# Kernel optimization log

Hardware: AMD Instinct MI355X
Metric: run time of the kernel (lower is better)

The kernel has to match this reference:

```python
import jax, jax.numpy as jnp
import numpy as np

N = 100000   # nodes
E = 640000   # edges
D = 128      # feature dim
G = 512      # graphs in the batch


def setup_inputs() -> dict:
    key = jax.random.key(0)
    ks = jax.random.split(key, 6)
    x = jax.random.normal(ks[0], (N, D), dtype=jnp.float32)
    edge_index = jax.random.randint(ks[1], (2, E), 0, N, dtype=jnp.int32)
    batch = jnp.sort(jax.random.randint(ks[2], (N,), 0, G, dtype=jnp.int32))
    scale = 1.0 / np.sqrt(D)
    W0 = jax.random.normal(ks[3], (D, D), dtype=jnp.float32) * scale
    W1 = jax.random.normal(ks[4], (D, D), dtype=jnp.float32) * scale
    W2 = jax.random.normal(ks[5], (D, D), dtype=jnp.float32) * scale
    return {"x": x, "edge_index": edge_index, "batch": batch,
            "W0": W0, "W1": W1, "W2": W2}


def gcn_conv(x, W, row, col, n):
    """GCNConv (bias=False): x' = D^-1/2 (A + I) D^-1/2 (x @ W).
    row/col already include self-loops."""
    xw = x @ W                                              # [N, D]
    deg = jax.ops.segment_sum(jnp.ones_like(col, dtype=x.dtype), col,
                              num_segments=n)               # [N]
    dinv = jnp.where(deg > 0, jax.lax.rsqrt(deg), 0.0)
    norm = dinv[row] * dinv[col]                            # [E+N]
    msgs = norm[:, None] * xw[row]                          # gather + scale
    return jax.ops.segment_sum(msgs, col, num_segments=n)   # scatter-add


def reference(x, edge_index, batch, W0, W1, W2):
    n = x.shape[0]
    loops = jnp.arange(n, dtype=edge_index.dtype)
    row = jnp.concatenate([edge_index[0], loops])
    col = jnp.concatenate([edge_index[1], loops])
    # conv_layers[:-1] (no activation between them in forward)
    x = gcn_conv(x, W0, row, col, n)
    x = gcn_conv(x, W1, row, col, n)
    x = jax.nn.leaky_relu(x, negative_slope=0.01)
    x = gcn_conv(x, W2, row, col, n)
    # global_add_pool over graph ids
    return jax.ops.segment_sum(x, batch, num_segments=G)    # [G, D]
```

## Files before the change

kernel.cpp:

```cpp
#include <hip/hip_runtime.h>
#include <hip/hip_bf16.h>

#define FEAT 128

typedef unsigned int uint32;
typedef unsigned long long uint64;
typedef unsigned short ushort16;
typedef __attribute__((ext_vector_type(8))) short short8;
typedef __attribute__((ext_vector_type(4))) float v4f;
typedef __attribute__((ext_vector_type(2))) float f32x2;

__device__ __forceinline__ ushort16 f2bf(float f) {
    uint32 u = __float_as_uint(f);
    u += 0x7fffu + ((u >> 16) & 1u);
    return (ushort16)(u >> 16);
}
__device__ __forceinline__ float bflo(uint32 u) { return __uint_as_float(u << 16); }
__device__ __forceinline__ float bfhi(uint32 u) { return __uint_as_float(u & 0xffff0000u); }
__device__ __forceinline__ f32x2 up2(uint32 u) { return (f32x2){bflo(u), bfhi(u)}; }

__global__ __launch_bounds__(256) void hydra_kernel(const float* __restrict__ x,
                                                    ushort16* __restrict__ Xh,
                                                    const int* __restrict__ col,
                                                    int* __restrict__ counts,
                                                    const float* __restrict__ W0,
                                                    const float* __restrict__ W1,
                                                    ushort16* __restrict__ W01t,
                                                    int cvtBlocks, int histBlocks,
                                                    int total8, int E) {
    int b = blockIdx.x;
    int t = threadIdx.x;
    if (b < cvtBlocks) {
        int id = b * 256 + t;
        if (id < total8) {
            const float4 v0 = *(const float4*)(x + (size_t)id * 8);
            const float4 v1 = *(const float4*)(x + (size_t)id * 8 + 4);
            uint4 o;
            o.x = (uint32)f2bf(v0.x) | ((uint32)f2bf(v0.y) << 16);
            o.y = (uint32)f2bf(v0.z) | ((uint32)f2bf(v0.w) << 16);
            o.z = (uint32)f2bf(v1.x) | ((uint32)f2bf(v1.y) << 16);
            o.w = (uint32)f2bf(v1.z) | ((uint32)f2bf(v1.w) << 16);
            *(uint4*)(Xh + (size_t)id * 8) = o;
        }
    } else if (b < cvtBlocks + histBlocks) {
        int id = (b - cvtBlocks) * 256 + t;
        if (id * 4 + 3 < E) {
            int4 c4 = *(const int4*)(col + id * 4);
            atomicAdd(&counts[c4.x], 1);
            atomicAdd(&counts[c4.y], 1);
            atomicAdd(&counts[c4.z], 1);
            atomicAdd(&counts[c4.w], 1);
        } else {
            for (int e = id * 4; e < E; e++) atomicAdd(&counts[col[e]], 1);
        }
    } else {
        __shared__ float sW0[2][FEAT];
        int wb = b - cvtBlocks - histBlocks;
        int lk = t >> 7;
        int ncol = t & 127;
        int k = wb * 2 + lk;
        sW0[lk][ncol] = W0[(size_t)k * FEAT + ncol];
        __syncthreads();
        float acc = 0.f;
#pragma unroll 4
        for (int j = 0; j < FEAT; j++)
            acc += sW0[lk][j] * W1[(size_t)j * FEAT + ncol];
        W01t[(size_t)ncol * FEAT + k] = f2bf(acc);
    }
}

__global__ __launch_bounds__(256) void scan_part(const int* __restrict__ counts,
                                                 int* __restrict__ bsum, int n) {
    __shared__ int s[256];
    int base = blockIdx.x * 1024;
    int t = threadIdx.x;
    int v = 0;
#pragma unroll
    for (int i = 0; i < 4; i++) {
        int idx = base + t * 4 + i;
        if (idx < n) v += counts[idx];
    }
    s[t] = v;
    __syncthreads();
    for (int o = 128; o > 0; o >>= 1) {
        if (t < o) s[t] += s[t + o];
        __syncthreads();
    }
    if (t == 0) bsum[blockIdx.x] = s[0];
}

__global__ void scan_bsum(int* __restrict__ bsum, int nb) {
    __shared__ int s[128];
    int t = threadIdx.x;
    int v0 = (t < nb) ? bsum[t] : 0;
    s[t] = v0;
    __syncthreads();
    for (int o = 1; o < 128; o <<= 1) {
        int v = (t >= o) ? s[t - o] : 0;
        __syncthreads();
        s[t] += v;
        __syncthreads();
    }
    if (t < nb) bsum[t] = s[t] - v0;
}

__global__ __launch_bounds__(256) void scan_final(const int* __restrict__ counts,
                                                  const int* __restrict__ bsum,
                                                  int* __restrict__ off, int* __restrict__ nxt,
                                                  float* __restrict__ dinv, int n) {
    __shared__ int s[256];
    int base = blockIdx.x * 1024;
    int t = threadIdx.x;
    int c[4];
    int sum = 0;
#pragma unroll
    for (int i = 0; i < 4; i++) {
        int idx = base + t * 4 + i;
        c[i] = (idx < n) ? counts[idx] : 0;
        sum += c[i];
    }
    int v0 = sum;
    s[t] = sum;
    __syncthreads();
    for (int o = 1; o < 256; o <<= 1) {
        int v = (t >= o) ? s[t - o] : 0;
        __syncthreads();
        s[t] += v;
        __syncthreads();
    }
    int excl = s[t] - v0 + bsum[blockIdx.x];
#pragma unroll
    for (int i = 0; i < 4; i++) {
        int idx = base + t * 4 + i;
        if (idx < n) {
            off[idx] = excl;
            nxt[idx] = excl;
            dinv[idx] = rsqrtf((float)(c[i] + 1));
        }
        excl += c[i];
    }
    if (blockIdx.x == gridDim.x - 1 && t == 255) off[n] = excl;
}

__global__ void fill_kernel(const int* __restrict__ row, const int* __restrict__ col,
                            const float* __restrict__ dinv, int* __restrict__ nxt,
                            uint64* __restrict__ erec, int E) {
    int e = blockIdx.x * 256 + threadIdx.x;
    if (e < E) {
        int c = col[e], r = row[e];
        int p = atomicAdd(&nxt[c], 1);
        uint64 v = (uint64)(uint32)r | ((uint64)__float_as_uint(dinv[r]) << 32);
        __builtin_nontemporal_store(v, &erec[p]);
    }
}

__global__ __launch_bounds__(256) void gemm_mfma(const ushort16* __restrict__ A,
                                                 const ushort16* __restrict__ Wt,
                                                 ushort16* __restrict__ Ch, int n,
                                                 int leaky) {
    const int t = threadIdx.x;
    const int w = t >> 6;
    const int lane = t & 63;
    const int quad = lane >> 4;
    const int l16 = lane & 15;
    const int colBase = (w & 1) * 64;

    short8 wf[4][4];
#pragma unroll
    for (int ct = 0; ct < 4; ct++) {
        const ushort16* wp = Wt + (size_t)(colBase + ct * 16 + l16) * FEAT + quad * 8;
#pragma unroll
        for (int ks = 0; ks < 4; ks++) wf[ct][ks] = *(const short8*)(wp + ks * 32);
    }

    const int nTiles = (n + 15) >> 4;
    const int tStride = gridDim.x * 2;
    int tile = blockIdx.x * 2 + (w >> 1);
    if (tile >= nTiles) return;

    auto loadA = [&](int tl, short8 (&a)[4]) {
        const int row = tl * 16 + l16;
        if (row < n) {
            const ushort16* ap = A + (size_t)row * FEAT + quad * 8;
#pragma unroll
            for (int ks = 0; ks < 4; ks++) a[ks] = *(const short8*)(ap + ks * 32);
        } else {
#pragma unroll
            for (int ks = 0; ks < 4; ks++) a[ks] = (short8)0;
        }
    };

    short8 aCur[4];
    loadA(tile, aCur);

    while (tile < nTiles) {
        const int nextTile = tile + tStride;
        short8 aNxt[4];
        if (nextTile < nTiles) loadA(nextTile, aNxt);

        v4f acc[4];
#pragma unroll
        for (int ct = 0; ct < 4; ct++) acc[ct] = (v4f)0.f;
#pragma unroll
        for (int ct = 0; ct < 4; ct++)
#pragma unroll
            for (int ks = 0; ks < 4; ks++)
                acc[ct] = __builtin_amdgcn_mfma_f32_16x16x32_bf16(wf[ct][ks], aCur[ks], acc[ct], 0, 0, 0);

        const int row = tile * 16 + l16;
        if (row < n) {
#pragma unroll
            for (int ct = 0; ct < 4; ct++) {
                float p0 = acc[ct][0], p1 = acc[ct][1], p2 = acc[ct][2], p3 = acc[ct][3];
                if (leaky) {
                    p0 = (p0 >= 0.f) ? p0 : 0.01f * p0;
                    p1 = (p1 >= 0.f) ? p1 : 0.01f * p1;
                    p2 = (p2 >= 0.f) ? p2 : 0.01f * p2;
                    p3 = (p3 >= 0.f) ? p3 : 0.01f * p3;
                }
                uint2 o;
                o.x = (uint32)f2bf(p0) | ((uint32)f2bf(p1) << 16);
                o.y = (uint32)f2bf(p2) | ((uint32)f2bf(p3) << 16);
                *(uint2*)(Ch + (size_t)row * FEAT + colBase + ct * 16 + quad * 4) = o;
            }
        }

        tile = nextTile;
#pragma unroll
        for (int ks = 0; ks < 4; ks++) aCur[ks] = aNxt[ks];
    }
}

__global__ __launch_bounds__(256) void gather_kernel(const int* __restrict__ off,
                                                     const uint2* __restrict__ erec,
                                                     const float* __restrict__ dinv,
                                                     const ushort16* __restrict__ XWh,
                                                     ushort16* __restrict__ Hh, int n) {
    int node = blockIdx.x * 4 + (threadIdx.x >> 6);
    if (node >= n) return;
    int lane = threadIdx.x & 63;
    int grp = lane >> 4;
    int l16 = lane & 15;
    float dc = dinv[node];
    const uint4* table = (const uint4*)XWh;

    f32x2 acc[4];
    if (grp == 0) {
        uint4 v = table[(size_t)node * 16 + l16];
        f32x2 w0 = (f32x2){dc * dc, dc * dc};
        acc[0] = w0 * up2(v.x);
        acc[1] = w0 * up2(v.y);
        acc[2] = w0 * up2(v.z);
        acc[3] = w0 * up2(v.w);
    } else {
#pragma unroll
        for (int j = 0; j < 4; j++) acc[j] = (f32x2){0.f, 0.f};
    }

    int s = off[node], e = off[node + 1];
    int i = s + grp;
    for (; i + 4 < e; i += 8) {
        uint2 er0 = erec[i];
        uint2 er1 = erec[i + 4];
        uint4 u0 = table[(size_t)er0.x * 16 + l16];
        uint4 u1 = table[(size_t)er1.x * 16 + l16];
        float f0 = dc * __uint_as_float(er0.y);
        float f1 = dc * __uint_as_float(er1.y);
        f32x2 n0 = (f32x2){f0, f0};
        f32x2 n1 = (f32x2){f1, f1};
        acc[0] += n0 * up2(u0.x);
        acc[1] += n0 * up2(u0.y);
        acc[2] += n0 * up2(u0.z);
        acc[3] += n0 * up2(u0.w);
        acc[0] += n1 * up2(u1.x);
        acc[1] += n1 * up2(u1.y);
        acc[2] += n1 * up2(u1.z);
        acc[3] += n1 * up2(u1.w);
    }
    if (i < e) {
        uint2 er0 = erec[i];
        uint4 u0 = table[(size_t)er0.x * 16 + l16];
        float f0 = dc * __uint_as_float(er0.y);
        f32x2 n0 = (f32x2){f0, f0};
        acc[0] += n0 * up2(u0.x);
        acc[1] += n0 * up2(u0.y);
        acc[2] += n0 * up2(u0.z);
        acc[3] += n0 * up2(u0.w);
    }

    float b[8] = {acc[0].x, acc[0].y, acc[1].x, acc[1].y,
                  acc[2].x, acc[2].y, acc[3].x, acc[3].y};
#pragma unroll
    for (int j = 0; j < 8; j++) {
        b[j] += __shfl_xor(b[j], 16);
        b[j] += __shfl_xor(b[j], 32);
    }

    if (grp == 0) {
        uint4 o;
        o.x = (uint32)f2bf(b[0]) | ((uint32)f2bf(b[1]) << 16);
        o.y = (uint32)f2bf(b[2]) | ((uint32)f2bf(b[3]) << 16);
        o.z = (uint32)f2bf(b[4]) | ((uint32)f2bf(b[5]) << 16);
        o.w = (uint32)f2bf(b[6]) | ((uint32)f2bf(b[7]) << 16);
        *(uint4*)(Hh + (size_t)node * FEAT + l16 * 8) = o;
    }
}

__global__ __launch_bounds__(128) void pool_kernel(const ushort16* __restrict__ H,
                                                   const int* __restrict__ batch,
                                                   float* __restrict__ P, int n) {
    int t = threadIdx.x;
    int i0 = blockIdx.x * 64;
    if (i0 >= n) return;
    int i1 = min(i0 + 64, n);
    float acc = 0.f;
    int g = batch[i0];
    for (int i = i0; i < i1; i++) {
        int b = batch[i];
        if (b != g) {
            atomicAdd(&P[(size_t)g * FEAT + t], acc);
            acc = 0.f;
            g = b;
        }
        uint32 u = (uint32)(unsigned short)H[(size_t)i * FEAT + t];
        acc += __uint_as_float(u << 16);
    }
    atomicAdd(&P[(size_t)g * FEAT + t], acc);
}

__global__ __launch_bounds__(128) void pgemm_kernel(const float* __restrict__ P,
                                                    const float* __restrict__ W2,
                                                    float* __restrict__ out) {
    __shared__ float sP[FEAT];
    const int g = blockIdx.x;
    const int t = threadIdx.x;
    sP[t] = P[(size_t)g * FEAT + t];
    __syncthreads();
    float o = 0.f;
#pragma unroll 4
    for (int k = 0; k < FEAT; k++) o += sP[k] * W2[(size_t)k * FEAT + t];
    out[(size_t)g * FEAT + t] = o;
}

extern "C" void kernel_launch(void* const* d_in, const int* in_sizes, int n_in,
                              void* d_out, int out_size, void* d_ws, size_t ws_size,
                              hipStream_t stream) {
    const float* x = (const float*)d_in[0];
    const int* ei = (const int*)d_in[1];
    const int* batch = (const int*)d_in[2];
    const float* W0 = (const float*)d_in[3];
    const float* W1 = (const float*)d_in[4];
    const float* W2 = (const float*)d_in[5];
    float* out = (float*)d_out;

    const int N = in_sizes[0] / FEAT;
    const int E = in_sizes[1] / 2;
    const int G = out_size / FEAT;

    const int* rowI = ei;
    const int* colI = ei + E;

    char* ws = (char*)d_ws;
    auto take = [&](size_t bytes) {
        char* p = ws;
        ws += (bytes + 15) & ~(size_t)15;
        return p;
    };
    int* counts    = (int*)take((size_t)N * 4);
    int* off       = (int*)take((size_t)(N + 1) * 4);
    int* nxt       = (int*)take((size_t)N * 4);
    float* dinv    = (float*)take((size_t)N * 4);
    int* bsum      = (int*)take(128 * 4);
    uint64* erec   = (uint64*)take((size_t)E * 8);
    ushort16* W01t = (ushort16*)take((size_t)16384 * 2);
    float* Pbuf    = (float*)take((size_t)G * FEAT * 4);
    ushort16* Xh   = (ushort16*)take((size_t)N * FEAT * 2);
    ushort16* bufA = (ushort16*)take((size_t)N * FEAT * 2);
    ushort16* bufB = (ushort16*)take((size_t)N * FEAT * 2);

    const int nb = (N + 1023) / 1024;
    const int eb = (E + 255) / 256;

    hipMemsetAsync(counts, 0, (size_t)N * 4, stream);
    hipMemsetAsync(Pbuf, 0, (size_t)G * FEAT * 4, stream);
    const int total8 = N * FEAT / 8;
    const int cvtBlocks = (total8 + 255) / 256;
    const int histBlocks = (E + 1023) / 1024;
    hydra_kernel<<<cvtBlocks + histBlocks + 64, 256, 0, stream>>>(
        x, Xh, colI, counts, W0, W1, W01t, cvtBlocks, histBlocks, total8, E);

    scan_part<<<nb, 256, 0, stream>>>(counts, bsum, N);
    scan_bsum<<<1, 128, 0, stream>>>(bsum, nb);
    scan_final<<<nb, 256, 0, stream>>>(counts, bsum, off, nxt, dinv, N);
    fill_kernel<<<eb, 256, 0, stream>>>(rowI, colI, dinv, nxt, erec, E);

    const int gatBlocks = (N + 3) / 4;

    gather_kernel<<<gatBlocks, 256, 0, stream>>>(off, (const uint2*)erec, dinv, Xh, bufA, N);
    gather_kernel<<<gatBlocks, 256, 0, stream>>>(off, (const uint2*)erec, dinv, bufA, bufB, N);
    gemm_mfma<<<1024, 256, 0, stream>>>(bufB, W01t, bufA, N, 1);
    gather_kernel<<<gatBlocks, 256, 0, stream>>>(off, (const uint2*)erec, dinv, bufA, bufB, N);
    pool_kernel<<<(N + 63) / 64, 128, 0, stream>>>(bufB, batch, Pbuf, N);
    pgemm_kernel<<<G, 128, 0, stream>>>(Pbuf, W2, out);
}
```

Baseline: 373.6 us.

## Drop scan_bsum and Pbuf memset launches, store source-only edge records

Folds the Pbuf zeroing into extra blocks of the hydra kernel, which removes a memset. It also removes the scan_bsum kernel by having each scan_final block sum the preceding block totals from shared memory. The edge records shrink from 8-byte (source, dinv) pairs to 4-byte source indices, and the gather kernels now read dinv[src] with a separate random load. This cuts kernel launches and halves edge-record traffic, at the cost of an extra dependent gather per edge in each of the three gather passes.

```diff
diff --git a/kernel.cpp b/kernel.cpp
--- a/kernel.cpp
+++ b/kernel.cpp
@@ -26,6 +26,7 @@
                                                     const float* __restrict__ W0,
                                                     const float* __restrict__ W1,
                                                     ushort16* __restrict__ W01t,
+                                                    float* __restrict__ Pbuf,
                                                     int cvtBlocks, int histBlocks,
                                                     int total8, int E) {
     int b = blockIdx.x;
@@ -53,7 +54,7 @@
         } else {
             for (int e = id * 4; e < E; e++) atomicAdd(&counts[col[e]], 1);
         }
-    } else {
+    } else if (b < cvtBlocks + histBlocks + 64) {
         __shared__ float sW0[2][FEAT];
         int wb = b - cvtBlocks - histBlocks;
         int lk = t >> 7;
@@ -66,6 +67,12 @@
         for (int j = 0; j < FEAT; j++)
             acc += sW0[lk][j] * W1[(size_t)j * FEAT + ncol];
         W01t[(size_t)ncol * FEAT + k] = f2bf(acc);
+    } else {
+        int zb = b - cvtBlocks - histBlocks - 64;
+        float4 z = make_float4(0.f, 0.f, 0.f, 0.f);
+        float* p = Pbuf + (size_t)zb * 2048 + t * 8;
+        *(float4*)p = z;
+        *(float4*)(p + 4) = z;
     }
 }
 
@@ -89,28 +96,15 @@
     if (t == 0) bsum[blockIdx.x] = s[0];
 }
 
-__global__ void scan_bsum(int* __restrict__ bsum, int nb) {
-    __shared__ int s[128];
-    int t = threadIdx.x;
-    int v0 = (t < nb) ? bsum[t] : 0;
-    s[t] = v0;
-    __syncthreads();
-    for (int o = 1; o < 128; o <<= 1) {
-        int v = (t >= o) ? s[t - o] : 0;
-        __syncthreads();
-        s[t] += v;
-        __syncthreads();
-    }
-    if (t < nb) bsum[t] = s[t] - v0;
-}
-
 __global__ __launch_bounds__(256) void scan_final(const int* __restrict__ counts,
                                                   const int* __restrict__ bsum,
                                                   int* __restrict__ off, int* __restrict__ nxt,
-                                                  float* __restrict__ dinv, int n) {
+                                                  float* __restrict__ dinv, int n, int nb) {
     __shared__ int s[256];
+    __shared__ int sb[128];
     int base = blockIdx.x * 1024;
     int t = threadIdx.x;
+    if (t < nb) sb[t] = bsum[t];
     int c[4];
     int sum = 0;
 #pragma unroll
@@ -128,7 +122,9 @@
         s[t] += v;
         __syncthreads();
     }
-    int excl = s[t] - v0 + bsum[blockIdx.x];
+    int blockBase = 0;
+    for (int j = 0; j < blockIdx.x; j++) blockBase += sb[j];
+    int excl = s[t] - v0 + blockBase;
 #pragma unroll
     for (int i = 0; i < 4; i++) {
         int idx = base + t * 4 + i;
@@ -143,14 +139,13 @@
 }
 
 __global__ void fill_kernel(const int* __restrict__ row, const int* __restrict__ col,
-                            const float* __restrict__ dinv, int* __restrict__ nxt,
-                            uint64* __restrict__ erec, int E) {
+                            int* __restrict__ nxt,
+                            int* __restrict__ srcArr, int E) {
     int e = blockIdx.x * 256 + threadIdx.x;
     if (e < E) {
         int c = col[e], r = row[e];
         int p = atomicAdd(&nxt[c], 1);
-        uint64 v = (uint64)(uint32)r | ((uint64)__float_as_uint(dinv[r]) << 32);
-        __builtin_nontemporal_store(v, &erec[p]);
+        __builtin_nontemporal_store(r, &srcArr[p]);
     }
 }
 
@@ -232,7 +227,7 @@
 }
 
 __global__ __launch_bounds__(256) void gather_kernel(const int* __restrict__ off,
-                                                     const uint2* __restrict__ erec,
+                                                     const int* __restrict__ srcArr,
                                                      const float* __restrict__ dinv,
                                                      const ushort16* __restrict__ XWh,
                                                      ushort16* __restrict__ Hh, int n) {
@@ -260,12 +255,12 @@
     int s = off[node], e = off[node + 1];
     int i = s + grp;
     for (; i + 4 < e; i += 8) {
-        uint2 er0 = erec[i];
-        uint2 er1 = erec[i + 4];
-        uint4 u0 = table[(size_t)er0.x * 16 + l16];
-        uint4 u1 = table[(size_t)er1.x * 16 + l16];
-        float f0 = dc * __uint_as_float(er0.y);
-        float f1 = dc * __uint_as_float(er1.y);
+        int r0 = srcArr[i];
+        int r1 = srcArr[i + 4];
+        uint4 u0 = table[(size_t)r0 * 16 + l16];
+        uint4 u1 = table[(size_t)r1 * 16 + l16];
+        float f0 = dc * dinv[r0];
+        float f1 = dc * dinv[r1];
         f32x2 n0 = (f32x2){f0, f0};
         f32x2 n1 = (f32x2){f1, f1};
         acc[0] += n0 * up2(u0.x);
@@ -278,9 +273,9 @@
         acc[3] += n1 * up2(u1.w);
     }
     if (i < e) {
-        uint2 er0 = erec[i];
-        uint4 u0 = table[(size_t)er0.x * 16 + l16];
-        float f0 = dc * __uint_as_float(er0.y);
+        int r0 = srcArr[i];
+        uint4 u0 = table[(size_t)r0 * 16 + l16];
+        float f0 = dc * dinv[r0];
         f32x2 n0 = (f32x2){f0, f0};
         acc[0] += n0 * up2(u0.x);
         acc[1] += n0 * up2(u0.y);
@@ -371,7 +366,7 @@
     int* nxt       = (int*)take((size_t)N * 4);
     float* dinv    = (float*)take((size_t)N * 4);
     int* bsum      = (int*)take(128 * 4);
-    uint64* erec   = (uint64*)take((size_t)E * 8);
+    int* srcArr    = (int*)take((size_t)E * 4);
     ushort16* W01t = (ushort16*)take((size_t)16384 * 2);
     float* Pbuf    = (float*)take((size_t)G * FEAT * 4);
     ushort16* Xh   = (ushort16*)take((size_t)N * FEAT * 2);
@@ -382,24 +377,22 @@
     const int eb = (E + 255) / 256;
 
     hipMemsetAsync(counts, 0, (size_t)N * 4, stream);
-    hipMemsetAsync(Pbuf, 0, (size_t)G * FEAT * 4, stream);
     const int total8 = N * FEAT / 8;
     const int cvtBlocks = (total8 + 255) / 256;
     const int histBlocks = (E + 1023) / 1024;
-    hydra_kernel<<<cvtBlocks + histBlocks + 64, 256, 0, stream>>>(
-        x, Xh, colI, counts, W0, W1, W01t, cvtBlocks, histBlocks, total8, E);
+    hydra_kernel<<<cvtBlocks + histBlocks + 64 + 32, 256, 0, stream>>>(
+        x, Xh, colI, counts, W0, W1, W01t, Pbuf, cvtBlocks, histBlocks, total8, E);
 
     scan_part<<<nb, 256, 0, stream>>>(counts, bsum, N);
-    scan_bsum<<<1, 128, 0, stream>>>(bsum, nb);
-    scan_final<<<nb, 256, 0, stream>>>(counts, bsum, off, nxt, dinv, N);
-    fill_kernel<<<eb, 256, 0, stream>>>(rowI, colI, dinv, nxt, erec, E);
+    scan_final<<<nb, 256, 0, stream>>>(counts, bsum, off, nxt, dinv, N, nb);
+    fill_kernel<<<eb, 256, 0, stream>>>(rowI, colI, nxt, srcArr, E);
 
     const int gatBlocks = (N + 3) / 4;
 
-    gather_kernel<<<gatBlocks, 256, 0, stream>>>(off, (const uint2*)erec, dinv, Xh, bufA, N);
-    gather_kernel<<<gatBlocks, 256, 0, stream>>>(off, (const uint2*)erec, dinv, bufA, bufB, N);
+    gather_kernel<<<gatBlocks, 256, 0, stream>>>(off, srcArr, dinv, Xh, bufA, N);
+    gather_kernel<<<gatBlocks, 256, 0, stream>>>(off, srcArr, dinv, bufA, bufB, N);
     gemm_mfma<<<1024, 256, 0, stream>>>(bufB, W01t, bufA, N, 1);
-    gather_kernel<<<gatBlocks, 256, 0, stream>>>(off, (const uint2*)erec, dinv, bufA, bufB, N);
+    gather_kernel<<<gatBlocks, 256, 0, stream>>>(off, srcArr, dinv, bufA, bufB, N);
     pool_kernel<<<(N + 63) / 64, 128, 0, stream>>>(bufB, batch, Pbuf, N);
     pgemm_kernel<<<G, 128, 0, stream>>>(Pbuf, W2, out);
 }
```

Measured after the change: 361.1 us. 3.4% less time.
